# Performance work log

Hardware: AMD Instinct MI355X
Metric: run time of the kernel (lower is better)

Reference implementation:

```python
import jax, jax.numpy as jnp
import numpy as np

B, N, CIN, COUT = 4, 4096, 64, 64

def setup_inputs() -> dict:
    key = jax.random.key(0)
    k1, k2, k3, k4, k5 = jax.random.split(key, 5)
    X = jax.random.normal(k1, (B, N, CIN), dtype=jnp.float32)
    A = jax.random.uniform(k2, (N, N), dtype=jnp.float32)
    weight1 = jax.random.normal(k3, (CIN, COUT), dtype=jnp.float32) * 0.05
    weight2 = jax.random.normal(k4, (1 * COUT, COUT), dtype=jnp.float32) * 0.05
    alpha = jax.random.normal(k5, (2 * COUT, 1), dtype=jnp.float32) * 0.05
    return {"X": X, "A": A, "weight1": weight1, "weight2": weight2, "alpha": alpha}

def reference(X, A, weight1, weight2, alpha):
    n = A.shape[0]
    c = weight1.shape[1]
    b = X.shape[0]
    # add self loops on the adjacency diagonal
    idx = jnp.arange(n)
    adj = A.at[idx, idx].set(1.0)
    # node transform: [B,N,C]
    out = jnp.matmul(X, weight1)
    # edge feature (P=1): [N,N,1], row-normalized over j (axis=1)
    E = adj[:, :, None]
    E_wave = E / E.sum(axis=1, keepdims=True)
    # attention scores via rank-1 decomposition of alpha
    att_l = jnp.matmul(out, alpha[:c])   # [B,N,1]
    att_r = jnp.matmul(out, alpha[c:])   # [B,N,1]
    scores = jax.nn.leaky_relu(att_l @ jnp.swapaxes(att_r, 1, 2))  # [B,N,N]
    # exp + edge-feature weighting: [P,B,N,N]
    att = jnp.einsum('bij,ijp->pbij', jnp.exp(scores), E_wave)
    # manual softmax-style normalization over neighbors j
    att = att / att.sum(axis=-1, keepdims=True)
    # aggregate: [B,N,P,C] -> [B,N,P*C]
    agg = jnp.einsum('pbij,bjc->bipc', att, out).reshape(b, n, -1)
    return jnp.matmul(agg, weight2)
```

## Files before the change

### kernel.cpp

```cpp
#include <hip/hip_runtime.h>
#include <hip/hip_bf16.h>

typedef __attribute__((ext_vector_type(8))) short short8;
typedef __attribute__((ext_vector_type(4))) float floatx4;

#define NN 4096

static __device__ __forceinline__ unsigned f2bf_rne(float x) {
    union { float f; unsigned u; } v; v.f = x;
    unsigned r = v.u + 0x7fffu + ((v.u >> 16) & 1u);
    return r >> 16;
}
static __device__ __forceinline__ float bf2f(unsigned hi) {
    union { unsigned u; float f; } v; v.u = hi << 16; return v.f;
}

__global__ __launch_bounds__(256, 4)
void prep_kernel(const float* __restrict__ X,
                 const float* __restrict__ W1,
                 const float* __restrict__ W2,
                 const float* __restrict__ alpha,
                 unsigned short* __restrict__ Gt,
                 float* __restrict__ lv,
                 float* __restrict__ rv) {
    __shared__ __align__(16) char sm[53248];
    float* W1s  = (float*)sm;
    float* W2s  = (float*)(sm + 17408);
    float* Wcst = (float*)(sm + 34816);
    float* w1s  = (float*)(sm + 52224);
    float* als  = (float*)(sm + 52736);
    float* GsT  = (float*)sm;

    const int t = threadIdx.x;
    const int row0 = blockIdx.x * 64;
    const int b = row0 >> 12, n0 = row0 & (NN - 1);
    const int w = t >> 6, lane = t & 63;
    const int m = lane & 15, q = lane >> 4;

    const int row = row0 + w * 16 + m;
    const float* xp = X + (size_t)row * 64;
    float4 x0 = *(const float4*)(xp + q * 8);
    float4 x1 = *(const float4*)(xp + q * 8 + 4);
    float4 x2 = *(const float4*)(xp + 32 + q * 8);
    float4 x3 = *(const float4*)(xp + 32 + q * 8 + 4);

    #pragma unroll
    for (int s = 0; s < 4; ++s) {
        int idx = s * 1024 + t * 4;
        int r = idx >> 6, cc = idx & 63;
        *(float4*)&W1s[r * 68 + cc] = *(const float4*)(W1 + idx);
        *(float4*)&W2s[r * 68 + cc] = *(const float4*)(W2 + idx);
    }
    if (t < 128) als[t] = alpha[t];
    __syncthreads();

    {
        const int k = t >> 2, nq = t & 3;
        float acc[16];
        #pragma unroll
        for (int i = 0; i < 16; ++i) acc[i] = 0.f;
        for (int mm = 0; mm < 64; ++mm) {
            float w1v = W1s[k * 68 + mm];
            #pragma unroll
            for (int i = 0; i < 16; ++i)
                acc[i] += w1v * W2s[mm * 68 + nq * 16 + i];
        }
        #pragma unroll
        for (int i = 0; i < 16; ++i)
            Wcst[(nq * 16 + i) * 68 + k] = acc[i];
    }
    if (t < 64) {
        float sl = 0.f, sr = 0.f;
        for (int cc2 = 0; cc2 < 64; ++cc2) {
            float wv = W1s[t * 68 + cc2];
            sl += wv * als[cc2];
            sr += wv * als[64 + cc2];
        }
        w1s[t] = sl; w1s[64 + t] = sr;
    }
    __syncthreads();

    const float xs[16] = {x0.x,x0.y,x0.z,x0.w, x1.x,x1.y,x1.z,x1.w,
                          x2.x,x2.y,x2.z,x2.w, x3.x,x3.y,x3.z,x3.w};

    float pl = 0.f, pr = 0.f;
    #pragma unroll
    for (int ks = 0; ks < 2; ++ks)
        #pragma unroll
        for (int j = 0; j < 8; ++j) {
            int k = ks * 32 + q * 8 + j;
            float xv = xs[ks * 8 + j];
            pl += xv * w1s[k];
            pr += xv * w1s[64 + k];
        }
    pl += __shfl_xor(pl, 16, 64); pl += __shfl_xor(pl, 32, 64);
    pr += __shfl_xor(pr, 16, 64); pr += __shfl_xor(pr, 32, 64);
    if (q == 0) { lv[row] = pl; rv[row] = pr; }

    short8 ah[2], al[2];
    #pragma unroll
    for (int ks = 0; ks < 2; ++ks)
        #pragma unroll
        for (int j = 0; j < 8; ++j) {
            float f = xs[ks * 8 + j];
            unsigned hb = f2bf_rne(f);
            float res = f - bf2f(hb);
            ah[ks][j] = (short)hb;
            al[ks][j] = (short)f2bf_rne(res);
        }

    short8 bfr[4][2];
    #pragma unroll
    for (int nt = 0; nt < 4; ++nt)
        #pragma unroll
        for (int ks = 0; ks < 2; ++ks) {
            const float* wp = &Wcst[(nt * 16 + m) * 68 + ks * 32 + q * 8];
            float4 w0 = *(const float4*)wp;
            float4 w1 = *(const float4*)(wp + 4);
            short8 bf;
            bf[0] = (short)f2bf_rne(w0.x); bf[1] = (short)f2bf_rne(w0.y);
            bf[2] = (short)f2bf_rne(w0.z); bf[3] = (short)f2bf_rne(w0.w);
            bf[4] = (short)f2bf_rne(w1.x); bf[5] = (short)f2bf_rne(w1.y);
            bf[6] = (short)f2bf_rne(w1.z); bf[7] = (short)f2bf_rne(w1.w);
            bfr[nt][ks] = bf;
        }

    floatx4 acc[4] = {{0,0,0,0},{0,0,0,0},{0,0,0,0},{0,0,0,0}};
    #pragma unroll
    for (int ks = 0; ks < 2; ++ks)
        #pragma unroll
        for (int nt = 0; nt < 4; ++nt) {
            acc[nt] = __builtin_amdgcn_mfma_f32_16x16x32_bf16(ah[ks], bfr[nt][ks], acc[nt], 0, 0, 0);
            acc[nt] = __builtin_amdgcn_mfma_f32_16x16x32_bf16(al[ks], bfr[nt][ks], acc[nt], 0, 0, 0);
        }

    __syncthreads();
    #pragma unroll
    for (int nt = 0; nt < 4; ++nt)
        #pragma unroll
        for (int rg = 0; rg < 4; ++rg)
            GsT[(nt * 16 + m) * 68 + w * 16 + q * 4 + rg] = acc[nt][rg];
    __syncthreads();
    unsigned* Gu = (unsigned*)Gt;
    #pragma unroll
    for (int it2 = 0; it2 < 8; ++it2) {
        int c2 = (t >> 5) + it2 * 8;
        int np = t & 31;
        unsigned lo = f2bf_rne(GsT[c2 * 68 + 2 * np]);
        unsigned hi = f2bf_rne(GsT[c2 * 68 + 2 * np + 1]);
        Gu[(((((size_t)(b * 64 + c2)) << 12) + n0) >> 1) + np] = lo | (hi << 16);
    }
}

__global__ __launch_bounds__(1024, 4)
void attn_kernel(const float* __restrict__ A,
                 const unsigned short* __restrict__ Gt,
                 const float* __restrict__ lv,
                 const float* __restrict__ rv,
                 float* __restrict__ out) {
    __shared__ __align__(16) char sm[57600];
    float* rs = (float*)sm;
    float* lis = (float*)(sm + 16384);
    unsigned short* Es = (unsigned short*)(sm + 16640);
    unsigned short* Gs = (unsigned short*)(sm + 37120);

    const int bx = blockIdx.x;
    const int i0 = (bx & 63) * 64;
    const int b  = bx >> 6;
    const int t = threadIdx.x;
    const int wave = t >> 6, lane = t & 63;
    const int grp = wave >> 2, wsub = wave & 3;
    const int m = lane & 15, q = lane >> 4;
    const int irow = wsub * 16 + (lane >> 2);
    const int jseg = lane & 3;

    *(float4*)&rs[t * 4] = *(const float4*)(rv + b * NN + t * 4);
    if (t < 64) lis[t] = lv[b * NN + i0 + t] * 1.44269504f;

    const float* aRow = A + (size_t)(i0 + irow) * NN + grp * 1024 + jseg * 8;
    const unsigned short* gRow = Gt + (((size_t)(b * 64 + irow)) << 12) + grp * 1024 + jseg * 8;
    const int jd = (i0 + irow) - grp * 1024;
    const bool diag_grp = (((i0 + irow) >> 10) == grp);

    unsigned short* EsG = Es + grp * 2560;
    unsigned short* GsG = Gs + grp * 2560;

    float4 a0A = *(const float4*)(aRow);
    float4 a1A = *(const float4*)(aRow + 4);
    uint4  gA  = *(const uint4*)(gRow);
    float4 a0B = *(const float4*)(aRow + 32);
    float4 a1B = *(const float4*)(aRow + 36);
    uint4  gB  = *(const uint4*)(gRow + 32);

    __syncthreads();
    const float li = lis[irow];

    floatx4 acc0 = {0,0,0,0}, acc1 = {0,0,0,0}, acc2 = {0,0,0,0},
            acc3 = {0,0,0,0}, accd = {0,0,0,0};
    short8 ones;
    #pragma unroll
    for (int e = 0; e < 8; ++e) ones[e] = (short)0x3F80;

    auto genE = [&](float4 a0, float4 a1, int chunk) -> uint4 {
        const int jl = chunk * 32 + jseg * 8;
        float aa[8] = {a0.x, a0.y, a0.z, a0.w, a1.x, a1.y, a1.z, a1.w};
        if (diag_grp && (jd >> 5) == chunk) {
            const int dd = jd - jl;
            #pragma unroll
            for (int e = 0; e < 8; ++e) if (dd == e) aa[e] = 1.0f;
        }
        const float4 r0 = *(const float4*)&rs[grp * 1024 + jl];
        const float4 r1 = *(const float4*)&rs[grp * 1024 + jl + 4];
        const float rr[8] = {r0.x, r0.y, r0.z, r0.w, r1.x, r1.y, r1.z, r1.w};
        unsigned ew[4];
        #pragma unroll
        for (int e2 = 0; e2 < 4; ++e2) {
            float s0 = li * rr[2 * e2], s1 = li * rr[2 * e2 + 1];
            s0 = fmaxf(s0, 0.01f * s0);
            s1 = fmaxf(s1, 0.01f * s1);
            float e0 = exp2f(s0) * aa[2 * e2];
            float e1 = exp2f(s1) * aa[2 * e2 + 1];
            ew[e2] = __builtin_amdgcn_perm(__float_as_uint(e1) + 0x8000u,
                                           __float_as_uint(e0) + 0x8000u, 0x07060302u);
        }
        return uint4{ew[0], ew[1], ew[2], ew[3]};
    };

    const int eoff = irow * 40 + jseg * 8;
    for (int c = 0; c < 32; c += 2) {
        uint4 eA = genE(a0A, a1A, c);
        uint4 gsvA = gA;
        { int jn = (c + 2 < 32) ? (c + 2) * 32 : c * 32;
          a0A = *(const float4*)(aRow + jn);
          a1A = *(const float4*)(aRow + jn + 4);
          gA  = *(const uint4*)(gRow + jn); }
        __syncthreads();
        *(uint4*)&EsG[eoff] = eA;
        *(uint4*)&GsG[eoff] = gsvA;
        __syncthreads();
        {
            short8 afr = *(const short8*)&EsG[(wsub * 16 + m) * 40 + q * 8];
            short8 b0  = *(const short8*)&GsG[(m)      * 40 + q * 8];
            short8 b1  = *(const short8*)&GsG[(16 + m) * 40 + q * 8];
            short8 b2  = *(const short8*)&GsG[(32 + m) * 40 + q * 8];
            short8 b3  = *(const short8*)&GsG[(48 + m) * 40 + q * 8];
            acc0 = __builtin_amdgcn_mfma_f32_16x16x32_bf16(afr, b0, acc0, 0, 0, 0);
            acc1 = __builtin_amdgcn_mfma_f32_16x16x32_bf16(afr, b1, acc1, 0, 0, 0);
            acc2 = __builtin_amdgcn_mfma_f32_16x16x32_bf16(afr, b2, acc2, 0, 0, 0);
            acc3 = __builtin_amdgcn_mfma_f32_16x16x32_bf16(afr, b3, acc3, 0, 0, 0);
            accd = __builtin_amdgcn_mfma_f32_16x16x32_bf16(afr, ones, accd, 0, 0, 0);
        }
        uint4 eB = genE(a0B, a1B, c + 1);
        uint4 gsvB = gB;
        { int jn = (c + 3 < 32) ? (c + 3) * 32 : (c + 1) * 32;
          a0B = *(const float4*)(aRow + jn);
          a1B = *(const float4*)(aRow + jn + 4);
          gB  = *(const uint4*)(gRow + jn); }
        __syncthreads();
        *(uint4*)&EsG[eoff] = eB;
        *(uint4*)&GsG[eoff] = gsvB;
        __syncthreads();
        {
            short8 afr = *(const short8*)&EsG[(wsub * 16 + m) * 40 + q * 8];
            short8 b0  = *(const short8*)&GsG[(m)      * 40 + q * 8];
            short8 b1  = *(const short8*)&GsG[(16 + m) * 40 + q * 8];
            short8 b2  = *(const short8*)&GsG[(32 + m) * 40 + q * 8];
            short8 b3  = *(const short8*)&GsG[(48 + m) * 40 + q * 8];
            acc0 = __builtin_amdgcn_mfma_f32_16x16x32_bf16(afr, b0, acc0, 0, 0, 0);
            acc1 = __builtin_amdgcn_mfma_f32_16x16x32_bf16(afr, b1, acc1, 0, 0, 0);
            acc2 = __builtin_amdgcn_mfma_f32_16x16x32_bf16(afr, b2, acc2, 0, 0, 0);
            acc3 = __builtin_amdgcn_mfma_f32_16x16x32_bf16(afr, b3, acc3, 0, 0, 0);
            accd = __builtin_amdgcn_mfma_f32_16x16x32_bf16(afr, ones, accd, 0, 0, 0);
        }
    }

    __syncthreads();
    float* red = (float*)sm;
    const int il = t >> 4, c4 = t & 15;
    float4 osum = {0.f, 0.f, 0.f, 0.f};
    float dsum = 0.f;
    #pragma unroll
    for (int pass = 0; pass < 2; ++pass) {
        if ((grp >> 1) == pass) {
            float* rp_ = red + (grp & 1) * 4352;
            #pragma unroll
            for (int nt = 0; nt < 4; ++nt) {
                floatx4 av = nt == 0 ? acc0 : nt == 1 ? acc1 : nt == 2 ? acc2 : acc3;
                #pragma unroll
                for (int rg = 0; rg < 4; ++rg)
                    rp_[(wsub * 16 + q * 4 + rg) * 68 + nt * 16 + m] = av[rg];
            }
            if (m == 0) {
                #pragma unroll
                for (int rg = 0; rg < 4; ++rg)
                    rp_[(wsub * 16 + q * 4 + rg) * 68 + 64] = accd[rg];
            }
        }
        __syncthreads();
        {
            float4 v0 = *(const float4*)&red[il * 68 + c4 * 4];
            float4 v1 = *(const float4*)&red[4352 + il * 68 + c4 * 4];
            osum.x += v0.x + v1.x; osum.y += v0.y + v1.y;
            osum.z += v0.z + v1.z; osum.w += v0.w + v1.w;
            dsum += red[il * 68 + 64] + red[4352 + il * 68 + 64];
        }
        __syncthreads();
    }
    const float rinv = 1.0f / dsum;
    float4 o;
    o.x = osum.x * rinv; o.y = osum.y * rinv;
    o.z = osum.z * rinv; o.w = osum.w * rinv;
    *(float4*)(out + (((size_t)(b * NN + i0 + il)) << 6) + c4 * 4) = o;
}

extern "C" void kernel_launch(void* const* d_in, const int* in_sizes, int n_in,
                              void* d_out, int out_size, void* d_ws, size_t ws_size,
                              hipStream_t stream) {
    const float* X     = (const float*)d_in[0];
    const float* A     = (const float*)d_in[1];
    const float* W1    = (const float*)d_in[2];
    const float* W2    = (const float*)d_in[3];
    const float* alpha = (const float*)d_in[4];
    float* out = (float*)d_out;

    char* ws = (char*)d_ws;
    unsigned short* Gt = (unsigned short*)(ws);
    float* lvp = (float*)(ws + 2097152);
    float* rvp = (float*)(ws + 2097152 + 65536);

    prep_kernel<<<256, 256, 0, stream>>>(X, W1, W2, alpha, Gt, lvp, rvp);
    attn_kernel<<<256, 1024, 0, stream>>>(A, Gt, lvp, rvp, out);
}
```

Before: 143.5 us.

## Load MFMA fragments directly from global, drop LDS staging and per-chunk barriers

```diff
diff --git a/kernel.cpp b/kernel.cpp
--- a/kernel.cpp
+++ b/kernel.cpp
@@ -158,60 +158,33 @@
                  const float* __restrict__ lv,
                  const float* __restrict__ rv,
                  float* __restrict__ out) {
-    __shared__ __align__(16) char sm[57600];
-    float* rs = (float*)sm;
-    float* lis = (float*)(sm + 16384);
-    unsigned short* Es = (unsigned short*)(sm + 16640);
-    unsigned short* Gs = (unsigned short*)(sm + 37120);
-
+    __shared__ __align__(16) float red[2][64][68];
     const int bx = blockIdx.x;
     const int i0 = (bx & 63) * 64;
     const int b  = bx >> 6;
     const int t = threadIdx.x;
     const int wave = t >> 6, lane = t & 63;
-    const int grp = wave >> 2, wsub = wave & 3;
+    const int wsub = wave & 1, jq = wave >> 1;
     const int m = lane & 15, q = lane >> 4;
-    const int irow = wsub * 16 + (lane >> 2);
-    const int jseg = lane & 3;
-
-    *(float4*)&rs[t * 4] = *(const float4*)(rv + b * NN + t * 4);
-    if (t < 64) lis[t] = lv[b * NN + i0 + t] * 1.44269504f;
-
-    const float* aRow = A + (size_t)(i0 + irow) * NN + grp * 1024 + jseg * 8;
-    const unsigned short* gRow = Gt + (((size_t)(b * 64 + irow)) << 12) + grp * 1024 + jseg * 8;
-    const int jd = (i0 + irow) - grp * 1024;
-    const bool diag_grp = (((i0 + irow) >> 10) == grp);
-
-    unsigned short* EsG = Es + grp * 2560;
-    unsigned short* GsG = Gs + grp * 2560;
-
-    float4 a0A = *(const float4*)(aRow);
-    float4 a1A = *(const float4*)(aRow + 4);
-    uint4  gA  = *(const uint4*)(gRow);
-    float4 a0B = *(const float4*)(aRow + 32);
-    float4 a1B = *(const float4*)(aRow + 36);
-    uint4  gB  = *(const uint4*)(gRow + 32);
-
-    __syncthreads();
-    const float li = lis[irow];
-
-    floatx4 acc0 = {0,0,0,0}, acc1 = {0,0,0,0}, acc2 = {0,0,0,0},
-            acc3 = {0,0,0,0}, accd = {0,0,0,0};
+
+    const int r0g = i0 + wsub * 32 + m;
+    const float li0 = lv[b * NN + r0g] * 1.44269504f;
+    const float li1 = lv[b * NN + r0g + 16] * 1.44269504f;
+
+    const float* a0p = A + (size_t)r0g * NN + jq * 512 + q * 8;
+    const float* a1p = a0p + (size_t)16 * NN;
+    const unsigned short* gp = Gt + (((size_t)(b * 64 + m)) << 12) + jq * 512 + q * 8;
+    const float* rvp = rv + b * NN + jq * 512 + q * 8;
+
+    floatx4 acc00 = {0,0,0,0}, acc01 = {0,0,0,0}, acc02 = {0,0,0,0}, acc03 = {0,0,0,0};
+    floatx4 acc10 = {0,0,0,0}, acc11 = {0,0,0,0}, acc12 = {0,0,0,0}, acc13 = {0,0,0,0};
+    floatx4 accd0 = {0,0,0,0}, accd1 = {0,0,0,0};
     short8 ones;
     #pragma unroll
     for (int e = 0; e < 8; ++e) ones[e] = (short)0x3F80;
 
-    auto genE = [&](float4 a0, float4 a1, int chunk) -> uint4 {
-        const int jl = chunk * 32 + jseg * 8;
-        float aa[8] = {a0.x, a0.y, a0.z, a0.w, a1.x, a1.y, a1.z, a1.w};
-        if (diag_grp && (jd >> 5) == chunk) {
-            const int dd = jd - jl;
-            #pragma unroll
-            for (int e = 0; e < 8; ++e) if (dd == e) aa[e] = 1.0f;
-        }
-        const float4 r0 = *(const float4*)&rs[grp * 1024 + jl];
-        const float4 r1 = *(const float4*)&rs[grp * 1024 + jl + 4];
-        const float rr[8] = {r0.x, r0.y, r0.z, r0.w, r1.x, r1.y, r1.z, r1.w};
+    auto genE = [&](float li, float4 a0, float4 a1, const float* rr) -> short8 {
+        const float aa[8] = {a0.x, a0.y, a0.z, a0.w, a1.x, a1.y, a1.z, a1.w};
         unsigned ew[4];
         #pragma unroll
         for (int e2 = 0; e2 < 4; ++e2) {
@@ -223,94 +196,118 @@
             ew[e2] = __builtin_amdgcn_perm(__float_as_uint(e1) + 0x8000u,
                                            __float_as_uint(e0) + 0x8000u, 0x07060302u);
         }
-        return uint4{ew[0], ew[1], ew[2], ew[3]};
+        union { uint4 u; short8 s; } pk;
+        pk.u.x = ew[0]; pk.u.y = ew[1]; pk.u.z = ew[2]; pk.u.w = ew[3];
+        return pk.s;
     };
 
-    const int eoff = irow * 40 + jseg * 8;
-    for (int c = 0; c < 32; c += 2) {
-        uint4 eA = genE(a0A, a1A, c);
-        uint4 gsvA = gA;
-        { int jn = (c + 2 < 32) ? (c + 2) * 32 : c * 32;
-          a0A = *(const float4*)(aRow + jn);
-          a1A = *(const float4*)(aRow + jn + 4);
-          gA  = *(const uint4*)(gRow + jn); }
-        __syncthreads();
-        *(uint4*)&EsG[eoff] = eA;
-        *(uint4*)&GsG[eoff] = gsvA;
-        __syncthreads();
-        {
-            short8 afr = *(const short8*)&EsG[(wsub * 16 + m) * 40 + q * 8];
-            short8 b0  = *(const short8*)&GsG[(m)      * 40 + q * 8];
-            short8 b1  = *(const short8*)&GsG[(16 + m) * 40 + q * 8];
-            short8 b2  = *(const short8*)&GsG[(32 + m) * 40 + q * 8];
-            short8 b3  = *(const short8*)&GsG[(48 + m) * 40 + q * 8];
-            acc0 = __builtin_amdgcn_mfma_f32_16x16x32_bf16(afr, b0, acc0, 0, 0, 0);
-            acc1 = __builtin_amdgcn_mfma_f32_16x16x32_bf16(afr, b1, acc1, 0, 0, 0);
-            acc2 = __builtin_amdgcn_mfma_f32_16x16x32_bf16(afr, b2, acc2, 0, 0, 0);
-            acc3 = __builtin_amdgcn_mfma_f32_16x16x32_bf16(afr, b3, acc3, 0, 0, 0);
-            accd = __builtin_amdgcn_mfma_f32_16x16x32_bf16(afr, ones, accd, 0, 0, 0);
-        }
-        uint4 eB = genE(a0B, a1B, c + 1);
-        uint4 gsvB = gB;
-        { int jn = (c + 3 < 32) ? (c + 3) * 32 : (c + 1) * 32;
-          a0B = *(const float4*)(aRow + jn);
-          a1B = *(const float4*)(aRow + jn + 4);
-          gB  = *(const uint4*)(gRow + jn); }
-        __syncthreads();
-        *(uint4*)&EsG[eoff] = eB;
-        *(uint4*)&GsG[eoff] = gsvB;
-        __syncthreads();
-        {
-            short8 afr = *(const short8*)&EsG[(wsub * 16 + m) * 40 + q * 8];
-            short8 b0  = *(const short8*)&GsG[(m)      * 40 + q * 8];
-            short8 b1  = *(const short8*)&GsG[(16 + m) * 40 + q * 8];
-            short8 b2  = *(const short8*)&GsG[(32 + m) * 40 + q * 8];
-            short8 b3  = *(const short8*)&GsG[(48 + m) * 40 + q * 8];
-            acc0 = __builtin_amdgcn_mfma_f32_16x16x32_bf16(afr, b0, acc0, 0, 0, 0);
-            acc1 = __builtin_amdgcn_mfma_f32_16x16x32_bf16(afr, b1, acc1, 0, 0, 0);
-            acc2 = __builtin_amdgcn_mfma_f32_16x16x32_bf16(afr, b2, acc2, 0, 0, 0);
-            acc3 = __builtin_amdgcn_mfma_f32_16x16x32_bf16(afr, b3, acc3, 0, 0, 0);
-            accd = __builtin_amdgcn_mfma_f32_16x16x32_bf16(afr, ones, accd, 0, 0, 0);
-        }
-    }
-
-    __syncthreads();
-    float* red = (float*)sm;
+    auto step = [&](int o, float4 x0, float4 x1, float4 y0, float4 y1,
+                    uint4 gu0, uint4 gu1, uint4 gu2, uint4 gu3) {
+        float4 rv0 = *(const float4*)(rvp + o);
+        float4 rv1 = *(const float4*)(rvp + o + 4);
+        const float rr[8] = {rv0.x, rv0.y, rv0.z, rv0.w, rv1.x, rv1.y, rv1.z, rv1.w};
+        short8 e0 = genE(li0, x0, x1, rr);
+        short8 e1 = genE(li1, y0, y1, rr);
+        union { uint4 u; short8 s; } g0, g1, g2, g3;
+        g0.u = gu0; g1.u = gu1; g2.u = gu2; g3.u = gu3;
+        acc00 = __builtin_amdgcn_mfma_f32_16x16x32_bf16(e0, g0.s, acc00, 0, 0, 0);
+        acc01 = __builtin_amdgcn_mfma_f32_16x16x32_bf16(e0, g1.s, acc01, 0, 0, 0);
+        acc02 = __builtin_amdgcn_mfma_f32_16x16x32_bf16(e0, g2.s, acc02, 0, 0, 0);
+        acc03 = __builtin_amdgcn_mfma_f32_16x16x32_bf16(e0, g3.s, acc03, 0, 0, 0);
+        accd0 = __builtin_amdgcn_mfma_f32_16x16x32_bf16(e0, ones, accd0, 0, 0, 0);
+        acc10 = __builtin_amdgcn_mfma_f32_16x16x32_bf16(e1, g0.s, acc10, 0, 0, 0);
+        acc11 = __builtin_amdgcn_mfma_f32_16x16x32_bf16(e1, g1.s, acc11, 0, 0, 0);
+        acc12 = __builtin_amdgcn_mfma_f32_16x16x32_bf16(e1, g2.s, acc12, 0, 0, 0);
+        acc13 = __builtin_amdgcn_mfma_f32_16x16x32_bf16(e1, g3.s, acc13, 0, 0, 0);
+        accd1 = __builtin_amdgcn_mfma_f32_16x16x32_bf16(e1, ones, accd1, 0, 0, 0);
+    };
+
+    #define LDCHUNK(o, X0, X1, Y0, Y1, G0, G1, G2, G3)                      \
+        X0 = *(const float4*)(a0p + (o));                                   \
+        X1 = *(const float4*)(a0p + (o) + 4);                               \
+        Y0 = *(const float4*)(a1p + (o));                                   \
+        Y1 = *(const float4*)(a1p + (o) + 4);                               \
+        G0 = *(const uint4*)(gp + (o));                                     \
+        G1 = *(const uint4*)(gp + (o) + (16 << 12));                        \
+        G2 = *(const uint4*)(gp + (o) + (32 << 12));                        \
+        G3 = *(const uint4*)(gp + (o) + (48 << 12));
+
+    float4 Ax0, Ax1, Ay0, Ay1; uint4 Ag0, Ag1, Ag2, Ag3;
+    float4 Bx0, Bx1, By0, By1; uint4 Bg0, Bg1, Bg2, Bg3;
+    LDCHUNK(0,  Ax0, Ax1, Ay0, Ay1, Ag0, Ag1, Ag2, Ag3);
+    LDCHUNK(32, Bx0, Bx1, By0, By1, Bg0, Bg1, Bg2, Bg3);
+
+    for (int jj = 0; jj < 512; jj += 64) {
+        float4 cx0 = Ax0, cx1 = Ax1, cy0 = Ay0, cy1 = Ay1;
+        uint4 cg0 = Ag0, cg1 = Ag1, cg2 = Ag2, cg3 = Ag3;
+        const int jn0 = (jj + 64 < 512) ? jj + 64 : jj;
+        LDCHUNK(jn0, Ax0, Ax1, Ay0, Ay1, Ag0, Ag1, Ag2, Ag3);
+        step(jj, cx0, cx1, cy0, cy1, cg0, cg1, cg2, cg3);
+
+        float4 dx0 = Bx0, dx1 = Bx1, dy0 = By0, dy1 = By1;
+        uint4 dg0 = Bg0, dg1 = Bg1, dg2 = Bg2, dg3 = Bg3;
+        const int jn1 = (jj + 96 < 512) ? jj + 96 : jj + 32;
+        LDCHUNK(jn1, Bx0, Bx1, By0, By1, Bg0, Bg1, Bg2, Bg3);
+        step(jj + 32, dx0, dx1, dy0, dy1, dg0, dg1, dg2, dg3);
+    }
+    #undef LDCHUNK
+
     const int il = t >> 4, c4 = t & 15;
     float4 osum = {0.f, 0.f, 0.f, 0.f};
     float dsum = 0.f;
     #pragma unroll
-    for (int pass = 0; pass < 2; ++pass) {
-        if ((grp >> 1) == pass) {
-            float* rp_ = red + (grp & 1) * 4352;
+    for (int p = 0; p < 4; ++p) {
+        if ((jq >> 1) == p) {
+            float (*rp)[68] = red[jq & 1];
             #pragma unroll
-            for (int nt = 0; nt < 4; ++nt) {
-                floatx4 av = nt == 0 ? acc0 : nt == 1 ? acc1 : nt == 2 ? acc2 : acc3;
-                #pragma unroll
-                for (int rg = 0; rg < 4; ++rg)
-                    rp_[(wsub * 16 + q * 4 + rg) * 68 + nt * 16 + m] = av[rg];
-            }
-            if (m == 0) {
-                #pragma unroll
-                for (int rg = 0; rg < 4; ++rg)
-                    rp_[(wsub * 16 + q * 4 + rg) * 68 + 64] = accd[rg];
+            for (int rg = 0; rg < 4; ++rg) {
+                const int r0l = wsub * 32 + q * 4 + rg;
+                rp[r0l][m]      = acc00[rg];
+                rp[r0l][16 + m] = acc01[rg];
+                rp[r0l][32 + m] = acc02[rg];
+                rp[r0l][48 + m] = acc03[rg];
+                rp[r0l + 16][m]      = acc10[rg];
+                rp[r0l + 16][16 + m] = acc11[rg];
+                rp[r0l + 16][32 + m] = acc12[rg];
+                rp[r0l + 16][48 + m] = acc13[rg];
+                if (m == 0) {
+                    rp[r0l][64]      = accd0[rg];
+                    rp[r0l + 16][64] = accd1[rg];
+                }
             }
         }
         __syncthreads();
         {
-            float4 v0 = *(const float4*)&red[il * 68 + c4 * 4];
-            float4 v1 = *(const float4*)&red[4352 + il * 68 + c4 * 4];
+            float4 v0 = *(const float4*)&red[0][il][c4 * 4];
+            float4 v1 = *(const float4*)&red[1][il][c4 * 4];
             osum.x += v0.x + v1.x; osum.y += v0.y + v1.y;
             osum.z += v0.z + v1.z; osum.w += v0.w + v1.w;
-            dsum += red[il * 68 + 64] + red[4352 + il * 68 + 64];
+            dsum += red[0][il][64] + red[1][il][64];
         }
         __syncthreads();
     }
+
+    const int gi = i0 + il;
+    {
+        float lir = lv[b * NN + gi] * 1.44269504f;
+        float rvi = rv[b * NN + gi];
+        float s = lir * rvi;
+        s = fmaxf(s, 0.01f * s);
+        float eii = exp2f(s);
+        float ad = A[(size_t)gi * NN + gi];
+        float dc = (1.0f - ad) * eii;
+        dsum += dc;
+        osum.x += dc * bf2f(Gt[(((size_t)(b * 64 + c4 * 4 + 0)) << 12) + gi]);
+        osum.y += dc * bf2f(Gt[(((size_t)(b * 64 + c4 * 4 + 1)) << 12) + gi]);
+        osum.z += dc * bf2f(Gt[(((size_t)(b * 64 + c4 * 4 + 2)) << 12) + gi]);
+        osum.w += dc * bf2f(Gt[(((size_t)(b * 64 + c4 * 4 + 3)) << 12) + gi]);
+    }
+
     const float rinv = 1.0f / dsum;
     float4 o;
     o.x = osum.x * rinv; o.y = osum.y * rinv;
     o.z = osum.z * rinv; o.w = osum.w * rinv;
-    *(float4*)(out + (((size_t)(b * NN + i0 + il)) << 6) + c4 * 4) = o;
+    *(float4*)(out + (((size_t)(b * NN + gi)) << 6) + c4 * 4) = o;
 }
 
 extern "C" void kernel_launch(void* const* d_in, const int* in_sizes, int n_in,
```

New measurement: 335.2 us. +133.5%, slower.
